# Kernel optimization log

Hardware: AMD Instinct MI355X
Metric: run time of the kernel (lower is better)

## Reference

```python
import jax, jax.numpy as jnp
import numpy as np

K = 9          # kernel_size (odd)
STRIDE = 1
EPS = 1e-12


def _unfold(x, k, stride, pad):
    # x: (bs, ch, H, W) -> (bs, ch, k, k, out_h, out_w); mimics F.unfold + view.
    bs, ch, H, W = x.shape
    out_h = (H + 2 * pad - k) // stride + 1
    out_w = (W + 2 * pad - k) // stride + 1
    xp = jnp.pad(x, ((0, 0), (0, 0), (pad, pad), (pad, pad)))
    rows = []
    for dy in range(k):  # fixed small loop over kernel taps
        row = [xp[:, :, dy:dy + out_h * stride:stride, dx:dx + out_w * stride:stride]
               for dx in range(k)]
        rows.append(jnp.stack(row, axis=2))
    return jnp.stack(rows, axis=2)


def setup_inputs() -> dict:
    key = jax.random.key(0)
    k1, k2 = jax.random.split(key)
    inp = jax.random.normal(k1, (2, 3, 384, 384), dtype=jnp.float32)
    sigmas = jax.random.uniform(k2, (2, 2, 384, 384), dtype=jnp.float32)
    return {"input": inp, "sigmas": sigmas}


def reference(input, sigmas):
    k, s = K, STRIDE
    pad = k // 2
    dt = input.dtype
    # inverse sigmas on strided grid
    sig_s = 1.0 / (jnp.abs(sigmas[:, 0:1, ::s, ::s]) + EPS)  # (bs,1,oh,ow)
    sig_r = 1.0 / (jnp.abs(sigmas[:, 1:2, ::s, ::s]) + EPS)
    # spatial Gaussian kernel, per-pixel sigma
    r = jnp.arange(-(k // 2), k // 2 + 1, dtype=dt)
    _1d = -0.5 * r * r
    _2d = (_1d[:, None] + _1d[None, :]).reshape(1, 1, k, k, 1, 1)
    g = jnp.exp(_2d * (sig_s * sig_s)[:, :, None, None, :, :])  # (bs,1,k,k,oh,ow)
    g = g / g.sum(axis=(2, 3), keepdims=True)
    # range (guide) Gaussian from local diff^2 summed over channels
    cols = _unfold(input, k, s, pad)                          # (bs,ch,k,k,oh,ow)
    center = cols[:, :, k // 2:k // 2 + 1, k // 2:k // 2 + 1]
    diff_sq = jnp.sum((cols - center) ** 2, axis=1, keepdims=True)
    guide = jnp.exp(-0.5 * diff_sq * (sig_r * sig_r)[:, :, None, None, :, :])
    # combine, normalize (guard empty windows), apply
    kmg = g * guide
    norm = kmg.sum(axis=(2, 3), keepdims=True)
    kmg = kmg / (norm + (norm == 0).astype(dt))
    out = jnp.sum(cols * kmg, axis=(2, 3))                    # (bs,ch,oh,ow)
    return out
```

## Files before the change

### kernel.cpp

```cpp
#include <hip/hip_runtime.h>
#include <hip/hip_bf16.h>

#define IMG_H 384
#define IMG_W 384
#define KSZ 9
#define KR 4
#define TILE 16
#define TIN (TILE + 2*KR)
#define LDS_STRIDE (TIN + 1)

__global__ __launch_bounds__(256) void abf_kernel(
    const float* __restrict__ input,
    const float* __restrict__ sigmas,
    float* __restrict__ out)
{
    __shared__ float s_in[3][TIN][LDS_STRIDE];

    const int b      = blockIdx.z;
    const int tile_x = blockIdx.x * TILE;
    const int tile_y = blockIdx.y * TILE;
    const int tx     = threadIdx.x;
    const int ty     = threadIdx.y;
    const int tid    = ty * TILE + tx;

    const float* inb = input + (size_t)b * 3 * IMG_H * IMG_W;
    for (int i = tid; i < 3 * TIN * TIN; i += 256) {
        int c   = i / (TIN * TIN);
        int rem = i - c * (TIN * TIN);
        int ly  = rem / TIN;
        int lx  = rem - ly * TIN;
        int gy  = tile_y + ly - KR;
        int gx  = tile_x + lx - KR;
        float v = 0.0f;
        if (gy >= 0 && gy < IMG_H && gx >= 0 && gx < IMG_W)
            v = inb[c * IMG_H * IMG_W + gy * IMG_W + gx];
        s_in[c][ly][lx] = v;
    }
    __syncthreads();

    const int ox = tile_x + tx;
    const int oy = tile_y + ty;

    const float* sgb = sigmas + (size_t)b * 2 * IMG_H * IMG_W;
    float sg0 = sgb[0 * IMG_H * IMG_W + oy * IMG_W + ox];
    float sg1 = sgb[1 * IMG_H * IMG_W + oy * IMG_W + ox];
    float sig_s = 1.0f / (fabsf(sg0) + 1e-12f);
    float sig_r = 1.0f / (fabsf(sg1) + 1e-12f);
    float ss2 = sig_s * sig_s;
    float sr2 = sig_r * sig_r;

    const float c0 = s_in[0][ty + KR][tx + KR];
    const float c1 = s_in[1][ty + KR][tx + KR];
    const float c2 = s_in[2][ty + KR][tx + KR];

    float acc0 = 0.0f, acc1 = 0.0f, acc2 = 0.0f, wsum = 0.0f;

    #pragma unroll
    for (int dy = 0; dy < KSZ; ++dy) {
        const float ry = (float)(dy - KR);
        const float sy = -0.5f * ry * ry;
        #pragma unroll
        for (int dx = 0; dx < KSZ; ++dx) {
            const float rx = (float)(dx - KR);
            const float sarg = (sy - 0.5f * rx * rx) * ss2;
            float v0 = s_in[0][ty + dy][tx + dx];
            float v1 = s_in[1][ty + dy][tx + dx];
            float v2 = s_in[2][ty + dy][tx + dx];
            float d0 = v0 - c0, d1 = v1 - c1, d2 = v2 - c2;
            float dsq = fmaf(d0, d0, fmaf(d1, d1, d2 * d2));
            float w = __expf(fmaf(-0.5f * dsq, sr2, sarg));
            wsum += w;
            acc0 = fmaf(w, v0, acc0);
            acc1 = fmaf(w, v1, acc1);
            acc2 = fmaf(w, v2, acc2);
        }
    }

    const float inv = 1.0f / wsum;
    float* outb = out + (size_t)b * 3 * IMG_H * IMG_W;
    outb[0 * IMG_H * IMG_W + oy * IMG_W + ox] = acc0 * inv;
    outb[1 * IMG_H * IMG_W + oy * IMG_W + ox] = acc1 * inv;
    outb[2 * IMG_H * IMG_W + oy * IMG_W + ox] = acc2 * inv;
}

extern "C" void kernel_launch(void* const* d_in, const int* in_sizes, int n_in,
                              void* d_out, int out_size, void* d_ws, size_t ws_size,
                              hipStream_t stream) {
    const float* input  = (const float*)d_in[0];
    const float* sigmas = (const float*)d_in[1];
    float* out = (float*)d_out;

    dim3 block(TILE, TILE, 1);
    dim3 grid(IMG_W / TILE, IMG_H / TILE, 2);
    abf_kernel<<<grid, block, 0, stream>>>(input, sigmas, out);
}
```

Baseline: 19.07 us.

## Pack channels into float4 LDS and use exp2 with folded constants

```diff
diff --git a/kernel.cpp b/kernel.cpp
--- a/kernel.cpp
+++ b/kernel.cpp
@@ -7,14 +7,15 @@
 #define KR 4
 #define TILE 16
 #define TIN (TILE + 2*KR)
-#define LDS_STRIDE (TIN + 1)
+#define SPX 25
+#define PLANE (IMG_H * IMG_W)
 
 __global__ __launch_bounds__(256) void abf_kernel(
     const float* __restrict__ input,
     const float* __restrict__ sigmas,
     float* __restrict__ out)
 {
-    __shared__ float s_in[3][TIN][LDS_STRIDE];
+    __shared__ float4 s_in[TIN * SPX];
 
     const int b      = blockIdx.z;
     const int tile_x = blockIdx.x * TILE;
@@ -23,64 +24,65 @@
     const int ty     = threadIdx.y;
     const int tid    = ty * TILE + tx;
 
-    const float* inb = input + (size_t)b * 3 * IMG_H * IMG_W;
-    for (int i = tid; i < 3 * TIN * TIN; i += 256) {
-        int c   = i / (TIN * TIN);
-        int rem = i - c * (TIN * TIN);
-        int ly  = rem / TIN;
-        int lx  = rem - ly * TIN;
-        int gy  = tile_y + ly - KR;
-        int gx  = tile_x + lx - KR;
-        float v = 0.0f;
-        if (gy >= 0 && gy < IMG_H && gx >= 0 && gx < IMG_W)
-            v = inb[c * IMG_H * IMG_W + gy * IMG_W + gx];
-        s_in[c][ly][lx] = v;
+    const float* inb = input + (size_t)b * 3 * PLANE;
+    for (int p = tid; p < TIN * TIN; p += 256) {
+        int py = p / TIN;
+        int px = p - py * TIN;
+        int gy = tile_y + py - KR;
+        int gx = tile_x + px - KR;
+        float4 v = make_float4(0.f, 0.f, 0.f, 0.f);
+        if (gy >= 0 && gy < IMG_H && gx >= 0 && gx < IMG_W) {
+            int gidx = gy * IMG_W + gx;
+            v.x = inb[gidx];
+            v.y = inb[PLANE + gidx];
+            v.z = inb[2 * PLANE + gidx];
+        }
+        s_in[py * SPX + px] = v;
     }
     __syncthreads();
 
     const int ox = tile_x + tx;
     const int oy = tile_y + ty;
 
-    const float* sgb = sigmas + (size_t)b * 2 * IMG_H * IMG_W;
-    float sg0 = sgb[0 * IMG_H * IMG_W + oy * IMG_W + ox];
-    float sg1 = sgb[1 * IMG_H * IMG_W + oy * IMG_W + ox];
-    float sig_s = 1.0f / (fabsf(sg0) + 1e-12f);
-    float sig_r = 1.0f / (fabsf(sg1) + 1e-12f);
-    float ss2 = sig_s * sig_s;
-    float sr2 = sig_r * sig_r;
+    const float* sgb = sigmas + (size_t)b * 2 * PLANE;
+    const float sg0 = sgb[oy * IMG_W + ox];
+    const float sg1 = sgb[PLANE + oy * IMG_W + ox];
+    const float sig_s = 1.0f / (fabsf(sg0) + 1e-12f);
+    const float sig_r = 1.0f / (fabsf(sg1) + 1e-12f);
+    const float A = -0.5f * 1.44269504f * sig_s * sig_s;
+    const float B = -0.5f * 1.44269504f * sig_r * sig_r;
 
-    const float c0 = s_in[0][ty + KR][tx + KR];
-    const float c1 = s_in[1][ty + KR][tx + KR];
-    const float c2 = s_in[2][ty + KR][tx + KR];
+    const float4 cen = s_in[(ty + KR) * SPX + (tx + KR)];
 
-    float acc0 = 0.0f, acc1 = 0.0f, acc2 = 0.0f, wsum = 0.0f;
+    float wsum = 1.0f;
+    float acc0 = cen.x, acc1 = cen.y, acc2 = cen.z;
 
     #pragma unroll
     for (int dy = 0; dy < KSZ; ++dy) {
-        const float ry = (float)(dy - KR);
-        const float sy = -0.5f * ry * ry;
+        const int base = (ty + dy) * SPX + tx;
         #pragma unroll
         for (int dx = 0; dx < KSZ; ++dx) {
-            const float rx = (float)(dx - KR);
-            const float sarg = (sy - 0.5f * rx * rx) * ss2;
-            float v0 = s_in[0][ty + dy][tx + dx];
-            float v1 = s_in[1][ty + dy][tx + dx];
-            float v2 = s_in[2][ty + dy][tx + dx];
-            float d0 = v0 - c0, d1 = v1 - c1, d2 = v2 - c2;
-            float dsq = fmaf(d0, d0, fmaf(d1, d1, d2 * d2));
-            float w = __expf(fmaf(-0.5f * dsq, sr2, sarg));
+            if (dy == KR && dx == KR) continue;
+            const float sc = (float)((dy - KR) * (dy - KR) + (dx - KR) * (dx - KR));
+            const float4 v = s_in[base + dx];
+            const float d0 = v.x - cen.x;
+            const float d1 = v.y - cen.y;
+            const float d2 = v.z - cen.z;
+            const float dsq = fmaf(d0, d0, fmaf(d1, d1, d2 * d2));
+            const float w = __builtin_amdgcn_exp2f(fmaf(dsq, B, sc * A));
             wsum += w;
-            acc0 = fmaf(w, v0, acc0);
-            acc1 = fmaf(w, v1, acc1);
-            acc2 = fmaf(w, v2, acc2);
+            acc0 = fmaf(w, v.x, acc0);
+            acc1 = fmaf(w, v.y, acc1);
+            acc2 = fmaf(w, v.z, acc2);
         }
     }
 
-    const float inv = 1.0f / wsum;
-    float* outb = out + (size_t)b * 3 * IMG_H * IMG_W;
-    outb[0 * IMG_H * IMG_W + oy * IMG_W + ox] = acc0 * inv;
-    outb[1 * IMG_H * IMG_W + oy * IMG_W + ox] = acc1 * inv;
-    outb[2 * IMG_H * IMG_W + oy * IMG_W + ox] = acc2 * inv;
+    const float inv = __builtin_amdgcn_rcpf(wsum);
+    float* outb = out + (size_t)b * 3 * PLANE;
+    const int oidx = oy * IMG_W + ox;
+    outb[oidx]             = acc0 * inv;
+    outb[PLANE + oidx]     = acc1 * inv;
+    outb[2 * PLANE + oidx] = acc2 * inv;
 }
 
 extern "C" void kernel_launch(void* const* d_in, const int* in_sizes, int n_in,
```

Measured after the change: 31.43 us. +64.8%, slower.
